# Kernel optimization log

Measured on AMD Instinct MI355X. Metric: run time of the kernel, lower is better.

## Reference

```python
import jax, jax.numpy as jnp
import numpy as np

D_MODEL = 512
D_INNER = 1024      # expand * d_model
NHEADS = 16         # d_inner // headdim, headdim = d_model // num_heads = 64
HEADDIM = 64
DSTATE = 64
DCONV = 4           # window_size
DFF = 2048
B, LM, LT = 16, 1024, 512


def _rmsnorm(x, eps=1e-6):
    return x * jax.lax.rsqrt(jnp.mean(x * x, axis=-1, keepdims=True) + eps)


def setup_inputs():
    key = jax.random.key(0)
    ks = jax.random.split(key, 10)
    conv_dim = D_INNER + 2 * DSTATE
    d_in_proj = 2 * D_INNER + 2 * DSTATE + NHEADS
    return {
        'tgt': jax.random.normal(ks[0], (B, LT, D_MODEL), jnp.float32),
        'memory': jax.random.normal(ks[1], (B, LM, D_MODEL), jnp.float32),
        'mem_mask': jnp.ones((B, LM), jnp.float32),
        'tgt_mask': jnp.ones((B, LT), jnp.float32),
        'in_proj_w': jax.random.normal(ks[2], (d_in_proj, D_MODEL), jnp.float32) * 0.02,
        'conv_w': jax.random.normal(ks[3], (conv_dim, DCONV), jnp.float32) * 0.2,
        'conv_b': jnp.zeros((conv_dim,), jnp.float32),
        'dt_bias': jax.random.uniform(ks[4], (NHEADS,), jnp.float32, -4.0, -2.0),
        'A_log': jnp.log(jax.random.uniform(ks[5], (NHEADS,), jnp.float32, 1.0, 16.0)),
        'D': jnp.ones((NHEADS,), jnp.float32),
        'norm_w': jnp.ones((D_INNER,), jnp.float32),
        'out_proj_w': jax.random.normal(ks[6], (D_MODEL, D_INNER), jnp.float32) * 0.02,
        'fc1_w': jax.random.normal(ks[7], (DFF, D_MODEL), jnp.float32) * 0.02,
        'fc1_b': jnp.zeros((DFF,), jnp.float32),
        'fc2_w': jax.random.normal(ks[8], (D_MODEL, DFF), jnp.float32) * 0.02,
        'fc2_b': jnp.zeros((D_MODEL,), jnp.float32),
    }


def _mamba2(u, in_proj_w, conv_w, conv_b, dt_bias, A_log, D, norm_w, out_proj_w):
    # u: (B, L, d_model) -- Mamba2-style selective scan (causal, ngroups=1)
    b, L, _ = u.shape
    zxbcdt = jnp.einsum('bld,ed->ble', u, in_proj_w)  # (B,L,2192)
    z = zxbcdt[..., :D_INNER]
    xBC = zxbcdt[..., D_INNER:D_INNER + D_INNER + 2 * DSTATE]
    dt = zxbcdt[..., -NHEADS:]

    # causal depthwise conv1d, kernel = DCONV, then swish
    xBC_pad = jnp.pad(xBC, ((0, 0), (DCONV - 1, 0), (0, 0)))
    conv = conv_b
    conv = sum(conv_w[:, k] * xBC_pad[:, k:k + L] for k in range(DCONV)) + conv_b
    xBC = jax.nn.silu(conv)

    x = xBC[..., :D_INNER].reshape(b, L, NHEADS, HEADDIM)   # (B,L,H,P)
    Bm = xBC[..., D_INNER:D_INNER + DSTATE]                  # (B,L,N)
    Cm = xBC[..., D_INNER + DSTATE:]                         # (B,L,N)

    dt = jax.nn.softplus(dt + dt_bias)                       # (B,L,H)
    A = -jnp.exp(A_log)                                      # (H,)
    a = jnp.exp(dt * A)                                      # (B,L,H) decay

    def step(h, inputs):
        a_t, dt_t, x_t, B_t, C_t = inputs
        # h: (B,H,P,N)
        h = a_t[:, :, None, None] * h + (dt_t[:, :, None] * x_t)[..., None] * B_t[:, None, None, :]
        y = jnp.einsum('bhpn,bn->bhp', h, C_t)
        return h, y

    h0 = jnp.zeros((b, NHEADS, HEADDIM, DSTATE), u.dtype)
    xs = (jnp.moveaxis(a, 1, 0), jnp.moveaxis(dt, 1, 0), jnp.moveaxis(x, 1, 0),
          jnp.moveaxis(Bm, 1, 0), jnp.moveaxis(Cm, 1, 0))
    _, ys = jax.lax.scan(step, h0, xs)                       # (L,B,H,P)
    y = jnp.moveaxis(ys, 0, 1) + D[None, None, :, None] * x  # skip term
    y = y.reshape(b, L, D_INNER)

    # gated RMSNorm + out_proj
    y = y * jax.nn.silu(z)
    y = _rmsnorm(y, 1e-5) * norm_w
    return jnp.einsum('ble,de->bld', y, out_proj_w)


def _forward(tgt, memory, mem_mask, tgt_mask, in_proj_w, conv_w, conv_b, dt_bias,
             A_log, D, norm_w, out_proj_w, fc1_w, fc1_b, fc2_w, fc2_b):
    tgt = tgt * tgt_mask[..., None]
    tgt1 = _rmsnorm(tgt)
    memory = memory * mem_mask[..., None]
    u = jnp.concatenate([memory, tgt1], axis=1)
    mask = jnp.concatenate([mem_mask, tgt_mask], axis=1)
    u = u * mask[..., None]
    tgt2 = _mamba2(u, in_proj_w, conv_w, conv_b, dt_bias, A_log, D, norm_w, out_proj_w)
    tgt2 = tgt2[:, -tgt1.shape[1]:]
    tgt = tgt + tgt2  # dropout = identity (eval)
    tgt1 = _rmsnorm(tgt)
    h = jax.nn.gelu(jnp.einsum('bld,fd->blf', tgt1, fc1_w) + fc1_b, approximate=False)
    tgt2 = jnp.einsum('blf,df->bld', h, fc2_w) + fc2_b
    return tgt + tgt2


def reference(tgt, memory, mem_mask, tgt_mask, in_proj_w, conv_w, conv_b, dt_bias,
              A_log, D, norm_w, out_proj_w, fc1_w, fc1_b, fc2_w, fc2_b):
    return _forward(tgt, memory, mem_mask, tgt_mask, in_proj_w, conv_w, conv_b, dt_bias,
                    A_log, D, norm_w, out_proj_w, fc1_w, fc1_b, fc2_w, fc2_b)
```

## Files before the change

### kernel.cpp

```cpp
#include <hip/hip_runtime.h>
#include <cstddef>

#define BB 16
#define LMM 1024
#define LTT 512
#define LL 1536
#define DMODEL 512
#define DINNER 1024
#define NH 16
#define DIPROJ 2192
#define DFF2 2048

typedef __bf16 bf16_t;
typedef bf16_t bf16x2 __attribute__((ext_vector_type(2)));
typedef bf16_t bf16x4 __attribute__((ext_vector_type(4)));
typedef bf16_t bf16x8 __attribute__((ext_vector_type(8)));
typedef float f32x4 __attribute__((ext_vector_type(4)));

typedef __attribute__((address_space(3))) void lds_void;
typedef const __attribute__((address_space(1))) void glb_void;

__device__ __forceinline__ void gload16(const void* g, void* l) {
  __builtin_amdgcn_global_load_lds((glb_void*)g, (lds_void*)l, 16, 0, 0);
}

__device__ inline float block_sum(float v, float* sbuf) {
#pragma unroll
  for (int off = 32; off > 0; off >>= 1) v += __shfl_xor(v, off, 64);
  int w = threadIdx.x >> 6;
  if ((threadIdx.x & 63) == 0) sbuf[w] = v;
  __syncthreads();
  return sbuf[0] + sbuf[1] + sbuf[2] + sbuf[3];
}

__global__ __launch_bounds__(256)
void cvt_w(const float* __restrict__ src, bf16_t* __restrict__ dst, int n)
{
  int i = (blockIdx.x * 256 + threadIdx.x) * 4;
  if (i < n) {
    float4 v = *(const float4*)&src[i];
    bf16x4 o;
    o[0] = (bf16_t)v.x; o[1] = (bf16_t)v.y; o[2] = (bf16_t)v.z; o[3] = (bf16_t)v.w;
    *(bf16x4*)&dst[i] = o;
  }
}

__global__ __launch_bounds__(256)
void prep_u(const float* __restrict__ tgt, const float* __restrict__ memory,
            const float* __restrict__ mem_mask, const float* __restrict__ tgt_mask,
            bf16_t* __restrict__ u, float* __restrict__ tgtm)
{
  __shared__ float sbuf[4];
  const int row = blockIdx.x;
  const int b = row / LL;
  const int t = row - b * LL;
  const int tid = threadIdx.x;
  if (t < LMM) {
    float m = mem_mask[b * LMM + t];
    float s = m * m;
    const float* src = memory + ((size_t)b * LMM + t) * DMODEL;
    float2 v = *(const float2*)&src[tid * 2];
    bf16x2 o; o[0] = (bf16_t)(v.x * s); o[1] = (bf16_t)(v.y * s);
    *(bf16x2*)&u[(size_t)row * DMODEL + tid * 2] = o;
  } else {
    const int tt = t - LMM;
    float mk = tgt_mask[b * LTT + tt];
    const float* src = tgt + ((size_t)b * LTT + tt) * DMODEL;
    float2 v = *(const float2*)&src[tid * 2];
    v.x *= mk; v.y *= mk;
    *(float2*)&tgtm[((size_t)b * LTT + tt) * DMODEL + tid * 2] = v;
    float ss = block_sum(v.x * v.x + v.y * v.y, sbuf);
    float inv = rsqrtf(ss * (1.0f / 512.0f) + 1e-6f) * mk;
    bf16x2 o; o[0] = (bf16_t)(v.x * inv); o[1] = (bf16_t)(v.y * inv);
    *(bf16x2*)&u[(size_t)row * DMODEL + tid * 2] = o;
  }
}

template<int EPI>
__global__ __launch_bounds__(256)
void gemm_abf(const bf16_t* __restrict__ A, const bf16_t* __restrict__ W,
              int M, int N, int K,
              float* __restrict__ Cf, bf16_t* __restrict__ Cb,
              const float* __restrict__ bias, const float* __restrict__ res,
              bf16_t* __restrict__ zbuf, bf16_t* __restrict__ xbc,
              float* __restrict__ dts, float* __restrict__ labuf,
              const float* __restrict__ dt_bias, const float* __restrict__ A_log)
{
  const int nbx = gridDim.x;
  const int nwg = nbx * gridDim.y;
  int flat = blockIdx.y * nbx + blockIdx.x;
  int swz = (flat & 7) * (nwg >> 3) + (flat >> 3);
  const int m0 = (swz / nbx) * 128;
  const int n0 = (swz % nbx) * 128;
  int bq = 0, tbase = 0;
  if (EPI == 4) {
    bq = m0 / LL; tbase = m0 - bq * LL;
    if (n0 + 128 <= DINNER && tbase < LMM) return;
  }
  __shared__ __align__(16) bf16_t As[2][128 * 64];
  __shared__ __align__(16) bf16_t Bs[2][128 * 64];
  const int tid = threadIdx.x;
  const int lane = tid & 63;
  const int wid = tid >> 6;
  const int wr = (wid >> 1) * 64, wc = (wid & 1) * 64;
  const int r = lane & 15;
  const int g = lane >> 4;
  const int r7 = r & 7;
  const int lrow = lane >> 3;
  const int sslot = (lane & 7) ^ lrow;

  int arow[4], brow[4];
#pragma unroll
  for (int ci = 0; ci < 4; ++ci) {
    int tr = wid * 32 + ci * 8 + lrow;
    arow[ci] = m0 + tr;
    int bn = n0 + tr;
    brow[ci] = bn < N ? bn : N - 1;
  }

  auto stage = [&](int buf, int kt) {
#pragma unroll
    for (int ci = 0; ci < 4; ++ci) {
      int chunk = wid * 4 + ci;
      gload16(A + (size_t)arow[ci] * K + kt + sslot * 8, &As[buf][chunk * 512]);
      gload16(W + (size_t)brow[ci] * K + kt + sslot * 8, &Bs[buf][chunk * 512]);
    }
  };

  f32x4 acc[4][4];
#pragma unroll
  for (int m = 0; m < 4; ++m)
#pragma unroll
    for (int n = 0; n < 4; ++n) acc[m][n] = (f32x4){0.f, 0.f, 0.f, 0.f};

  const int NK = K >> 6;
  stage(0, 0);
  __syncthreads();
  for (int ki = 0; ki < NK; ++ki) {
    const int cur = ki & 1;
    if (ki + 1 < NK) stage(cur ^ 1, (ki + 1) << 6);
#pragma unroll
    for (int c = 0; c < 2; ++c) {
      bf16x8 af[4], bfr[4];
#pragma unroll
      for (int m = 0; m < 4; ++m) {
        int row = wr + m * 16 + r;
        af[m] = *(const bf16x8*)&As[cur][row * 64 + (((c * 4 + g) ^ r7) * 8)];
      }
#pragma unroll
      for (int n = 0; n < 4; ++n) {
        int row = wc + n * 16 + r;
        bfr[n] = *(const bf16x8*)&Bs[cur][row * 64 + (((c * 4 + g) ^ r7) * 8)];
      }
#pragma unroll
      for (int m = 0; m < 4; ++m)
#pragma unroll
        for (int n = 0; n < 4; ++n)
          acc[m][n] = __builtin_amdgcn_mfma_f32_16x16x32_bf16(af[m], bfr[n], acc[m][n], 0, 0, 0);
    }
    if (ki + 1 < NK) __syncthreads();
  }

#pragma unroll
  for (int m = 0; m < 4; ++m) {
#pragma unroll
    for (int n = 0; n < 4; ++n) {
      int gcol = n0 + wc + n * 16 + r;
      if (gcol >= N) continue;
#pragma unroll
      for (int j = 0; j < 4; ++j) {
        float v = acc[m][n][j];
        if (EPI == 4) {
          int t = tbase + wr + m * 16 + g * 4 + j;
          if (gcol < DINNER) {
            zbuf[(((size_t)(bq * LTT + t - LMM)) << 10) + gcol] = (bf16_t)v;
          } else if (gcol < DINNER + 1152) {
            xbc[(size_t)(bq * LL + t) * 1152 + (gcol - DINNER)] = (bf16_t)v;
          } else {
            int h = gcol - 2176;
            float raw = v + dt_bias[h];
            float d = raw > 20.f ? raw : log1pf(expf(raw));
            size_t ix = (size_t)(bq * LL + t) * 16 + h;
            dts[ix] = d;
            labuf[ix] = -expf(A_log[h]) * d;
          }
        } else {
          int grow = m0 + wr + m * 16 + g * 4 + j;
          if (EPI == 1) {
            v += bias[gcol];
            v = 0.5f * v * (1.f + erff(v * 0.70710678f));
            Cb[(size_t)grow * N + gcol] = (bf16_t)v;
          } else if (EPI == 2) {
            v += bias[gcol] + res[(size_t)grow * N + gcol];
            Cf[(size_t)grow * N + gcol] = v;
          } else {
            v += res[(size_t)grow * N + gcol];
            Cf[(size_t)grow * N + gcol] = v;
          }
        }
      }
    }
  }
}

__global__ __launch_bounds__(256)
void sbc_k(const bf16_t* __restrict__ xbc, const float* __restrict__ cw,
           const float* __restrict__ cb, bf16_t* __restrict__ BtG,
           bf16_t* __restrict__ Sg, bf16_t* __restrict__ CcG)
{
  __shared__ __align__(16) bf16_t rawBC[132 * 128];
  __shared__ __align__(16) bf16_t CB[128 * 128];
  __shared__ float wls[128 * 4];
  __shared__ float bls[128];
  const int c = blockIdx.x, b = blockIdx.y;
  const int t0 = c * 128;
  const int tid = threadIdx.x, lane = tid & 63, wid = tid >> 6;
  const int r = lane & 15, g = lane >> 4;

  if (tid < 128) {
    int gch = 1024 + tid;
#pragma unroll
    for (int k = 0; k < 4; ++k) wls[tid * 4 + k] = cw[gch * 4 + k];
    bls[tid] = cb[gch];
  }
#pragma unroll
  for (int ci = 0; ci < 9; ++ci) {
    int chunk = ci * 4 + wid;
    if (chunk < 33) {
      int F = chunk * 1024 + lane * 16;
      int row = F >> 8, off = F & 255;
      gload16(xbc + (size_t)(b * LL + t0 - 3 + row) * 1152 + 1024 + off / 2,
              &rawBC[chunk * 512]);
    }
  }
  __syncthreads();
  if (c == 0 && tid < 48) {
    bf16x8 z;
#pragma unroll
    for (int j = 0; j < 8; ++j) z[j] = (bf16_t)0.f;
    *(bf16x8*)&rawBC[tid * 8] = z;
  }
  __syncthreads();
#pragma unroll 2
  for (int it = 0; it < 64; ++it) {
    int o = tid + it * 256;
    int t = o >> 7, ch = o & 127;
    float a0 = bls[ch];
#pragma unroll
    for (int kk = 0; kk < 4; ++kk)
      a0 = fmaf(wls[ch * 4 + kk], (float)rawBC[(t + kk) * 128 + ch], a0);
    float sv = a0 / (1.f + expf(-a0));
    int slot = ch >> 3;
    int swslot = (slot & 8) | ((slot & 7) ^ (t & 7));
    CB[t * 128 + swslot * 8 + (ch & 7)] = (bf16_t)sv;
    if (c >= 8 && ch >= 64) {
      int n = ch - 64;
      CcG[(((size_t)(b * 4 + (c - 8)) * 128 + t)) * 64 + (((n >> 3) ^ (t & 7)) << 3) + (n & 7)] = (bf16_t)sv;
    }
  }
  __syncthreads();
  {
    int n = tid & 63, tb = tid >> 6;
#pragma unroll
    for (int s8 = 0; s8 < 4; ++s8) {
      int ts = tb * 32 + s8 * 8;
      bf16x8 v;
#pragma unroll
      for (int e = 0; e < 8; ++e) {
        int t = ts + e;
        int slot = (n >> 3) ^ (t & 7);
        v[e] = CB[t * 128 + slot * 8 + (n & 7)];
      }
      *(bf16x8*)&BtG[((size_t)(b * 12 + c) * 64 + n) * 128 + ((((ts >> 3) ^ (n & 7))) << 3)] = v;
    }
  }
  if (c >= 8) {
    f32x4 sacc[2][8];
#pragma unroll
    for (int tt = 0; tt < 2; ++tt)
#pragma unroll
      for (int ct = 0; ct < 8; ++ct) sacc[tt][ct] = (f32x4){0.f, 0.f, 0.f, 0.f};
    const int ctn = 2 * wid + 2;
#pragma unroll
    for (int kk = 0; kk < 2; ++kk) {
      bf16x8 ca[2];
#pragma unroll
      for (int tt = 0; tt < 2; ++tt) {
        int trow = wid * 32 + tt * 16 + r;
        int slot = (64 + kk * 32 + g * 8) >> 3;
        int sw = (slot & 8) | ((slot & 7) ^ (trow & 7));
        ca[tt] = *(const bf16x8*)&CB[trow * 128 + sw * 8];
      }
#pragma unroll
      for (int ct = 0; ct < 8; ++ct) {
        if (ct < ctn) {
          int taur = ct * 16 + r;
          int sw = ((kk * 4 + g) ^ (taur & 7));
          bf16x8 bb = *(const bf16x8*)&CB[taur * 128 + sw * 8];
          sacc[0][ct] = __builtin_amdgcn_mfma_f32_16x16x32_bf16(ca[0], bb, sacc[0][ct], 0, 0, 0);
          sacc[1][ct] = __builtin_amdgcn_mfma_f32_16x16x32_bf16(ca[1], bb, sacc[1][ct], 0, 0, 0);
        }
      }
    }
    size_t sbase = (size_t)(b * 4 + (c - 8)) * 16384;
#pragma unroll
    for (int tt = 0; tt < 2; ++tt)
#pragma unroll
      for (int ct = 0; ct < 8; ++ct) {
        if (ct < ctn) {
#pragma unroll
          for (int j = 0; j < 4; ++j) {
            int ta = wid * 32 + tt * 16 + g * 4 + j;
            int tau = ct * 16 + r;
            Sg[sbase + ta * 128 + (tau ^ ((ta & 7) << 3))] = (bf16_t)sacc[tt][ct][j];
          }
        }
      }
  }
}

__global__ __launch_bounds__(256)
void ssd_hend(const bf16_t* __restrict__ xbc, const float* __restrict__ dts,
              const float* __restrict__ labuf, const float* __restrict__ cw,
              const float* __restrict__ cb, const bf16_t* __restrict__ BtG,
              bf16_t* __restrict__ hend, float* __restrict__ Lacum,
              float* __restrict__ Ak)
{
  __shared__ __align__(16) bf16_t rawX[136 * 64];
  __shared__ __align__(16) bf16_t Xt[64 * 128];
  __shared__ __align__(16) bf16_t Bt[64 * 128];
  __shared__ float wv[128];
  __shared__ float wls[64 * 4];
  __shared__ float bls[64];
  const int c = blockIdx.x;
  const int bh = blockIdx.y;
  const int b = bh >> 4, h = bh & 15;
  const int t0 = c * 128;
  const int tid = threadIdx.x, lane = tid & 63, wid = tid >> 6;
  const int r = lane & 15, g = lane >> 4;

  if (tid < 64) {
    int gch = h * 64 + tid;
#pragma unroll
    for (int k = 0; k < 4; ++k) wls[tid * 4 + k] = cw[gch * 4 + k];
    bls[tid] = cb[gch];
  }
#pragma unroll
  for (int ci = 0; ci < 5; ++ci) {
    int chunk = ci * 4 + wid;
    if (chunk < 17) {
      int F = chunk * 1024 + lane * 16;
      int row = F >> 7, off = F & 127;
      gload16(xbc + (size_t)(b * LL + t0 - 3 + row) * 1152 + h * 64 + off / 2,
              &rawX[chunk * 512]);
    }
  }
#pragma unroll
  for (int ci = 0; ci < 4; ++ci) {
    int chunk = ci * 4 + wid;
    int F = chunk * 1024 + lane * 16;
    gload16(BtG + (size_t)(b * 12 + c) * 8192 + F / 2, &Bt[chunk * 512]);
  }
  __syncthreads();
  if (c == 0 && tid < 24) {
    bf16x8 z;
#pragma unroll
    for (int j = 0; j < 8; ++j) z[j] = (bf16_t)0.f;
    *(bf16x8*)&rawX[tid * 8] = z;
  }
  if (tid < 64) {
    float v0 = labuf[(size_t)(b * LL + t0 + tid) * 16 + h];
    float v1 = labuf[(size_t)(b * LL + t0 + 64 + tid) * 16 + h];
    float d0 = dts[(size_t)(b * LL + t0 + tid) * 16 + h];
    float d1 = dts[(size_t)(b * LL + t0 + 64 + tid) * 16 + h];
#pragma unroll
    for (int d = 1; d < 64; d <<= 1) { float t_ = __shfl(v0, tid - d, 64); if (tid >= d) v0 += t_; }
    float T0 = __shfl(v0, 63, 64);
#pragma unroll
    for (int d = 1; d < 64; d <<= 1) { float t_ = __shfl(v1, tid - d, 64); if (tid >= d) v1 += t_; }
    v1 += T0;
    float Ls = __shfl(v1, 63, 64);
    wv[tid] = expf(Ls - v0) * d0; wv[64 + tid] = expf(Ls - v1) * d1;
    Lacum[(size_t)(bh * 12 + c) * 128 + tid] = v0;
    Lacum[(size_t)(bh * 12 + c) * 128 + 64 + tid] = v1;
    if (tid == 0) Ak[bh * 12 + c] = expf(Ls);
  }
  __syncthreads();
  {
    int p = tid & 63, tb = (tid >> 6) * 32;
    float w0 = wls[p * 4], w1 = wls[p * 4 + 1], w2 = wls[p * 4 + 2], w3 = wls[p * 4 + 3];
    float bb0 = bls[p];
    int sw = (p & 7) << 3;
#pragma unroll
    for (int i8 = 0; i8 < 4; ++i8) {
      bf16x8 ov;
#pragma unroll
      for (int e = 0; e < 8; ++e) {
        int t = tb + i8 * 8 + e;
        float a0 = bb0;
        a0 = fmaf(w0, (float)rawX[(t + 0) * 64 + p], a0);
        a0 = fmaf(w1, (float)rawX[(t + 1) * 64 + p], a0);
        a0 = fmaf(w2, (float)rawX[(t + 2) * 64 + p], a0);
        a0 = fmaf(w3, (float)rawX[(t + 3) * 64 + p], a0);
        ov[e] = (bf16_t)(a0 / (1.f + expf(-a0)));
      }
      *(bf16x8*)&Xt[p * 128 + ((tb + i8 * 8) ^ sw)] = ov;
    }
  }
  __syncthreads();
  f32x4 acc[4];
#pragma unroll
  for (int n = 0; n < 4; ++n) acc[n] = (f32x4){0.f, 0.f, 0.f, 0.f};
  const int prow = wid * 16 + r;
#pragma unroll
  for (int kk = 0; kk < 4; ++kk) {
    int k0 = kk * 32 + g * 8;
    bf16x8 xv = *(const bf16x8*)&Xt[prow * 128 + (k0 ^ ((prow & 7) << 3))];
    bf16x8 af;
#pragma unroll
    for (int j = 0; j < 8; ++j) af[j] = (bf16_t)((float)xv[j] * wv[k0 + j]);
#pragma unroll
    for (int nt = 0; nt < 4; ++nt) {
      int nrow = nt * 16 + r;
      bf16x8 bf_ = *(const bf16x8*)&Bt[nrow * 128 + (k0 ^ ((nrow & 7) << 3))];
      acc[nt] = __builtin_amdgcn_mfma_f32_16x16x32_bf16(af, bf_, acc[nt], 0, 0, 0);
    }
  }
  size_t base = ((size_t)(bh * 12 + c)) * 4096;
#pragma unroll
  for (int nt = 0; nt < 4; ++nt)
#pragma unroll
    for (int j = 0; j < 4; ++j)
      hend[base + (size_t)(wid * 16 + g * 4 + j) * 64 + nt * 16 + r] = (bf16_t)acc[nt][j];
}

__global__ __launch_bounds__(256)
void ssd_y(const bf16_t* __restrict__ xbc, const float* __restrict__ dts,
           const bf16_t* __restrict__ hend, const float* __restrict__ Ak,
           const float* __restrict__ Lacum, const bf16_t* __restrict__ Sg,
           const bf16_t* __restrict__ CcG, const float* __restrict__ cw,
           const float* __restrict__ cb, const float* __restrict__ Dp,
           bf16_t* __restrict__ ybuf)
{
  __shared__ __align__(16) char region0[32768];
  __shared__ __align__(16) bf16_t Xt[64 * 128];
  __shared__ __align__(16) bf16_t Cs[128 * 64];
  __shared__ __align__(16) bf16_t hts[64 * 64];
  __shared__ float Lat[128];
  __shared__ float dtv[128];
  __shared__ float wls[64 * 4];
  __shared__ float bls[64];
  bf16_t* rawX = (bf16_t*)region0;
  bf16_t* Gs   = (bf16_t*)region0;
  const int c = 8 + blockIdx.x;
  const int bh = blockIdx.y;
  const int b = bh >> 4, h = bh & 15;
  const int t0 = c * 128;
  const int tid = threadIdx.x, lane = tid & 63, wid = tid >> 6;
  const int r = lane & 15, g = lane >> 4;

  if (tid < 64) {
    int gch = h * 64 + tid;
#pragma unroll
    for (int k = 0; k < 4; ++k) wls[tid * 4 + k] = cw[gch * 4 + k];
    bls[tid] = cb[gch];
  }
  if (tid < 128) {
    Lat[tid] = Lacum[(size_t)(bh * 12 + c) * 128 + tid];
    dtv[tid] = dts[(size_t)(b * LL + t0 + tid) * 16 + h];
  }
#pragma unroll
  for (int ci = 0; ci < 5; ++ci) {
    int chunk = ci * 4 + wid;
    if (chunk < 17) {
      int F = chunk * 1024 + lane * 16;
      int row = F >> 7, off = F & 127;
      gload16(xbc + (size_t)(b * LL + t0 - 3 + row) * 1152 + h * 64 + off / 2,
              &rawX[chunk * 512]);
    }
  }
#pragma unroll
  for (int ci = 0; ci < 4; ++ci) {
    int chunk = ci * 4 + wid;
    int F = chunk * 1024 + lane * 16;
    gload16(CcG + (size_t)(b * 4 + (c - 8)) * 8192 + F / 2, &Cs[chunk * 512]);
  }
  {
    float hin[16];
#pragma unroll
    for (int e = 0; e < 16; ++e) hin[e] = 0.f;
    float accp = 1.f;
    for (int k = c - 1; k >= 0; --k) {
      const bf16_t* hp = hend + ((size_t)(bh * 12 + k)) * 4096 + tid * 16;
      bf16x8 e0 = *(const bf16x8*)hp;
      bf16x8 e1 = *(const bf16x8*)(hp + 8);
#pragma unroll
      for (int j = 0; j < 8; ++j) {
        hin[j]     = fmaf(accp, (float)e0[j], hin[j]);
        hin[j + 8] = fmaf(accp, (float)e1[j], hin[j + 8]);
      }
      accp *= Ak[bh * 12 + k];
    }
    int p = tid >> 2, n0 = (tid & 3) * 16;
    bf16x8 o0, o1;
#pragma unroll
    for (int j = 0; j < 8; ++j) { o0[j] = (bf16_t)hin[j]; o1[j] = (bf16_t)hin[j + 8]; }
    int p7 = p & 7;
    *(bf16x8*)&hts[p * 64 + (((n0 >> 3) ^ p7) << 3)] = o0;
    *(bf16x8*)&hts[p * 64 + ((((n0 >> 3) + 1) ^ p7) << 3)] = o1;
  }
  __syncthreads();
  {
    int p = tid & 63, tb = (tid >> 6) * 32;
    float w0 = wls[p * 4], w1 = wls[p * 4 + 1], w2 = wls[p * 4 + 2], w3 = wls[p * 4 + 3];
    float bb0 = bls[p];
    int sw = (p & 7) << 3;
#pragma unroll
    for (int i8 = 0; i8 < 4; ++i8) {
      bf16x8 ov;
#pragma unroll
      for (int e = 0; e < 8; ++e) {
        int t = tb + i8 * 8 + e;
        float a0 = bb0;
        a0 = fmaf(w0, (float)rawX[(t + 0) * 64 + p], a0);
        a0 = fmaf(w1, (float)rawX[(t + 1) * 64 + p], a0);
        a0 = fmaf(w2, (float)rawX[(t + 2) * 64 + p], a0);
        a0 = fmaf(w3, (float)rawX[(t + 3) * 64 + p], a0);
        ov[e] = (bf16_t)(a0 / (1.f + expf(-a0)));
      }
      *(bf16x8*)&Xt[p * 128 + ((tb + i8 * 8) ^ sw)] = ov;
    }
  }
  __syncthreads();
  {
    size_t sbase = (size_t)(b * 4 + (c - 8)) * 16384;
#pragma unroll
    for (int it = 0; it < 8; ++it) {
      int o = tid + it * 256;
      int ta = o >> 4, sl = o & 15;
      bf16x8 sv = *(const bf16x8*)&Sg[sbase + ta * 128 + sl * 8];
      int tau0 = (sl ^ (ta & 7)) * 8;
      float Lta = Lat[ta];
      bf16x8 gv;
#pragma unroll
      for (int e = 0; e < 8; ++e) {
        int tau = tau0 + e;
        float xa = (tau <= ta) ? (Lta - Lat[tau]) : -1e30f;
        gv[e] = (bf16_t)(expf(xa) * dtv[tau] * (float)sv[e]);
      }
      *(bf16x8*)&Gs[ta * 128 + sl * 8] = gv;
    }
  }
  __syncthreads();

  bf16x8 caf[2][2];
#pragma unroll
  for (int tt = 0; tt < 2; ++tt)
#pragma unroll
    for (int kk = 0; kk < 2; ++kk) {
      int trow = wid * 32 + tt * 16 + r;
      caf[tt][kk] = *(const bf16x8*)&Cs[trow * 64 + ((((kk * 4 + g)) ^ (trow & 7)) << 3)];
    }

  f32x4 accY[2][4], acc2[2][4];
#pragma unroll
  for (int tt = 0; tt < 2; ++tt)
#pragma unroll
    for (int pt = 0; pt < 4; ++pt) {
      accY[tt][pt] = (f32x4){0.f, 0.f, 0.f, 0.f};
      acc2[tt][pt] = (f32x4){0.f, 0.f, 0.f, 0.f};
    }
#pragma unroll
  for (int tt = 0; tt < 2; ++tt) {
    int trow = wid * 32 + tt * 16 + r;
#pragma unroll
    for (int kk = 0; kk < 4; ++kk) {
      if (kk <= wid) {
        int k0 = kk * 32 + g * 8;
        bf16x8 ga = *(const bf16x8*)&Gs[trow * 128 + (k0 ^ ((trow & 7) << 3))];
#pragma unroll
        for (int pt = 0; pt < 4; ++pt) {
          int prow = pt * 16 + r;
          bf16x8 xb = *(const bf16x8*)&Xt[prow * 128 + (k0 ^ ((prow & 7) << 3))];
          accY[tt][pt] = __builtin_amdgcn_mfma_f32_16x16x32_bf16(ga, xb, accY[tt][pt], 0, 0, 0);
        }
      }
    }
#pragma unroll
    for (int kk = 0; kk < 2; ++kk) {
#pragma unroll
      for (int pt = 0; pt < 4; ++pt) {
        int prow = pt * 16 + r;
        bf16x8 hb = *(const bf16x8*)&hts[prow * 64 + ((((kk * 4 + g)) ^ (prow & 7)) << 3)];
        acc2[tt][pt] = __builtin_amdgcn_mfma_f32_16x16x32_bf16(caf[tt][kk], hb, acc2[tt][pt], 0, 0, 0);
      }
    }
  }

  const float Dh = Dp[h];
#pragma unroll
  for (int tt = 0; tt < 2; ++tt) {
#pragma unroll
    for (int j = 0; j < 4; ++j) {
      int trow = wid * 32 + tt * 16 + g * 4 + j;
      float el = expf(Lat[trow]);
      size_t yrow = ((size_t)(b * LTT + (c - 8) * 128 + trow)) << 10;
#pragma unroll
      for (int pt = 0; pt < 4; ++pt) {
        int p = pt * 16 + r;
        float xv = (float)Xt[p * 128 + (trow ^ ((p & 7) << 3))];
        float yv = accY[tt][pt][j] + el * acc2[tt][pt][j] + Dh * xv;
        ybuf[yrow + h * 64 + p] = (bf16_t)yv;
      }
    }
  }
}

__global__ __launch_bounds__(256)
void gate_norm_k(const bf16_t* __restrict__ zbuf, const bf16_t* __restrict__ ybuf,
                 const float* __restrict__ norm_w, bf16_t* __restrict__ yn)
{
  __shared__ float sbuf[4];
  const int row = blockIdx.x;
  const int tid = threadIdx.x;
  bf16x4 yv = *(const bf16x4*)&ybuf[(size_t)row * DINNER + tid * 4];
  bf16x4 zv = *(const bf16x4*)&zbuf[(size_t)row * DINNER + tid * 4];
  float v[4];
#pragma unroll
  for (int c = 0; c < 4; ++c) {
    float y = (float)yv[c], z = (float)zv[c];
    v[c] = y * (z / (1.f + expf(-z)));
  }
  float ss = block_sum(v[0]*v[0] + v[1]*v[1] + v[2]*v[2] + v[3]*v[3], sbuf);
  float inv = rsqrtf(ss * (1.f / 1024.f) + 1e-5f);
  float4 nw = *(const float4*)&norm_w[tid * 4];
  bf16x4 o;
  o[0] = (bf16_t)(v[0] * inv * nw.x); o[1] = (bf16_t)(v[1] * inv * nw.y);
  o[2] = (bf16_t)(v[2] * inv * nw.z); o[3] = (bf16_t)(v[3] * inv * nw.w);
  *(bf16x4*)&yn[(size_t)row * DINNER + tid * 4] = o;
}

__global__ __launch_bounds__(256)
void rms_k(const float* __restrict__ in, bf16_t* __restrict__ out)
{
  __shared__ float sbuf[4];
  const int row = blockIdx.x;
  const int tid = threadIdx.x;
  float2 v = *(const float2*)&in[(size_t)row * DMODEL + tid * 2];
  float ss = block_sum(v.x * v.x + v.y * v.y, sbuf);
  float inv = rsqrtf(ss * (1.f / 512.f) + 1e-6f);
  bf16x2 o; o[0] = (bf16_t)(v.x * inv); o[1] = (bf16_t)(v.y * inv);
  *(bf16x2*)&out[(size_t)row * DMODEL + tid * 2] = o;
}

extern "C" void kernel_launch(void* const* d_in, const int* in_sizes, int n_in,
                              void* d_out, int out_size, void* d_ws, size_t ws_size,
                              hipStream_t stream)
{
  const float* tgt        = (const float*)d_in[0];
  const float* memory     = (const float*)d_in[1];
  const float* mem_mask   = (const float*)d_in[2];
  const float* tgt_mask   = (const float*)d_in[3];
  const float* in_proj_w  = (const float*)d_in[4];
  const float* conv_w     = (const float*)d_in[5];
  const float* conv_b     = (const float*)d_in[6];
  const float* dt_bias    = (const float*)d_in[7];
  const float* A_log      = (const float*)d_in[8];
  const float* Dp         = (const float*)d_in[9];
  const float* norm_w     = (const float*)d_in[10];
  const float* out_proj_w = (const float*)d_in[11];
  const float* fc1_w      = (const float*)d_in[12];
  const float* fc1_b      = (const float*)d_in[13];
  const float* fc2_w      = (const float*)d_in[14];
  const float* fc2_b      = (const float*)d_in[15];

  char* wsb = (char*)d_ws;
  bf16_t* u     = (bf16_t*)(wsb + 0);
  bf16_t* zbuf  = (bf16_t*)(wsb + 25165824);
  bf16_t* xbc   = (bf16_t*)(wsb + 41943040);
  float*  dts   = (float*)(wsb + 98566144);
  float*  labuf = (float*)(wsb + 100139008);
  float*  tgtm  = (float*)(wsb + 101711872);
  bf16_t* hend  = (bf16_t*)(wsb + 118489088);
  float*  Lacum = (float*)(wsb + 143667200);
  float*  Akb   = (float*)(wsb + 145240064);
  bf16_t* BtG   = (bf16_t*)(wsb + 145252352);
  bf16_t* Sg    = (bf16_t*)(wsb + 148398080);
  bf16_t* CcG   = (bf16_t*)(wsb + 150495232);
  bf16_t* wip   = (bf16_t*)(wsb + 160444416);
  bf16_t* wop   = wip + 1122304;
  bf16_t* wf1   = wop + 524288;
  bf16_t* wf2   = wf1 + 1048576;
  bf16_t* ybuf  = (bf16_t*)(wsb + 0);
  bf16_t* yn    = (bf16_t*)(wsb + 41943040);
  float*  tres  = (float*)(wsb + 58720256);
  bf16_t* t1    = (bf16_t*)(wsb + 75497472);
  bf16_t* hbuf  = (bf16_t*)(wsb + 0);
  float* outp = (float*)d_out;

  cvt_w<<<1096, 256, 0, stream>>>(in_proj_w, wip, 1122304);
  cvt_w<<<512, 256, 0, stream>>>(out_proj_w, wop, 524288);
  cvt_w<<<1024, 256, 0, stream>>>(fc1_w, wf1, 1048576);
  cvt_w<<<1024, 256, 0, stream>>>(fc2_w, wf2, 1048576);
  prep_u<<<BB * LL, 256, 0, stream>>>(tgt, memory, mem_mask, tgt_mask, u, tgtm);
  gemm_abf<4><<<dim3(18, 192), 256, 0, stream>>>(u, wip, BB * LL, DIPROJ, DMODEL,
      nullptr, nullptr, nullptr, nullptr, zbuf, xbc, dts, labuf, dt_bias, A_log);
  sbc_k<<<dim3(12, BB), 256, 0, stream>>>(xbc, conv_w, conv_b, BtG, Sg, CcG);
  ssd_hend<<<dim3(12, BB * NH), 256, 0, stream>>>(xbc, dts, labuf, conv_w, conv_b,
      BtG, hend, Lacum, Akb);
  ssd_y<<<dim3(4, BB * NH), 256, 0, stream>>>(xbc, dts, hend, Akb, Lacum, Sg, CcG,
      conv_w, conv_b, Dp, ybuf);
  gate_norm_k<<<BB * LTT, 256, 0, stream>>>(zbuf, ybuf, norm_w, yn);
  gemm_abf<3><<<dim3(4, 64), 256, 0, stream>>>(yn, wop, BB * LTT, DMODEL, DINNER,
      tres, nullptr, nullptr, tgtm, nullptr, nullptr, nullptr, nullptr, nullptr, nullptr);
  rms_k<<<BB * LTT, 256, 0, stream>>>(tres, t1);
  gemm_abf<1><<<dim3(16, 64), 256, 0, stream>>>(t1, wf1, BB * LTT, DFF2, DMODEL,
      nullptr, hbuf, fc1_b, nullptr, nullptr, nullptr, nullptr, nullptr, nullptr, nullptr);
  gemm_abf<2><<<dim3(4, 64), 256, 0, stream>>>(hbuf, wf2, BB * LTT, DMODEL, DFF2,
      outp, nullptr, fc2_b, tres, nullptr, nullptr, nullptr, nullptr, nullptr, nullptr);
}
```

Before: 338.6 us.

## Load GEMM fragments directly from global memory and merge weight conversion kernels

Replaces the LDS double-buffered GEMM staging with direct per-lane global loads of MFMA fragments, so shared memory and all __syncthreads disappear. The four weight-conversion launches become one kernel. A t>=LMM guard is added to the z-buffer write in the in_proj epilogue. Without LDS reuse, every wave fetches its A and B rows independently through cache, which raises global/L2 traffic and exposes memory latency with no explicit prefetching.

```diff
diff --git a/kernel.cpp b/kernel.cpp
--- a/kernel.cpp
+++ b/kernel.cpp
@@ -34,15 +34,22 @@
 }
 
 __global__ __launch_bounds__(256)
-void cvt_w(const float* __restrict__ src, bf16_t* __restrict__ dst, int n)
+void cvt_all(const float* __restrict__ s0, const float* __restrict__ s1,
+             const float* __restrict__ s2, const float* __restrict__ s3,
+             bf16_t* __restrict__ dst)
 {
   int i = (blockIdx.x * 256 + threadIdx.x) * 4;
-  if (i < n) {
-    float4 v = *(const float4*)&src[i];
-    bf16x4 o;
-    o[0] = (bf16_t)v.x; o[1] = (bf16_t)v.y; o[2] = (bf16_t)v.z; o[3] = (bf16_t)v.w;
-    *(bf16x4*)&dst[i] = o;
-  }
+  if (i >= 3743744) return;
+  const float* src;
+  int off;
+  if (i < 1122304)      { src = s0; off = i; }
+  else if (i < 1646592) { src = s1; off = i - 1122304; }
+  else if (i < 2695168) { src = s2; off = i - 1646592; }
+  else                  { src = s3; off = i - 2695168; }
+  float4 v = *(const float4*)&src[off];
+  bf16x4 o;
+  o[0] = (bf16_t)v.x; o[1] = (bf16_t)v.y; o[2] = (bf16_t)v.z; o[3] = (bf16_t)v.w;
+  *(bf16x4*)&dst[i] = o;
 }
 
 __global__ __launch_bounds__(256)
@@ -78,7 +85,7 @@
 
 template<int EPI>
 __global__ __launch_bounds__(256)
-void gemm_abf(const bf16_t* __restrict__ A, const bf16_t* __restrict__ W,
+void gemm_dir(const bf16_t* __restrict__ A, const bf16_t* __restrict__ W,
               int M, int N, int K,
               float* __restrict__ Cf, bf16_t* __restrict__ Cb,
               const float* __restrict__ bias, const float* __restrict__ res,
@@ -97,35 +104,24 @@
     bq = m0 / LL; tbase = m0 - bq * LL;
     if (n0 + 128 <= DINNER && tbase < LMM) return;
   }
-  __shared__ __align__(16) bf16_t As[2][128 * 64];
-  __shared__ __align__(16) bf16_t Bs[2][128 * 64];
   const int tid = threadIdx.x;
   const int lane = tid & 63;
   const int wid = tid >> 6;
   const int wr = (wid >> 1) * 64, wc = (wid & 1) * 64;
   const int r = lane & 15;
   const int g = lane >> 4;
-  const int r7 = r & 7;
-  const int lrow = lane >> 3;
-  const int sslot = (lane & 7) ^ lrow;
-
-  int arow[4], brow[4];
-#pragma unroll
-  for (int ci = 0; ci < 4; ++ci) {
-    int tr = wid * 32 + ci * 8 + lrow;
-    arow[ci] = m0 + tr;
-    int bn = n0 + tr;
-    brow[ci] = bn < N ? bn : N - 1;
-  }
-
-  auto stage = [&](int buf, int kt) {
-#pragma unroll
-    for (int ci = 0; ci < 4; ++ci) {
-      int chunk = wid * 4 + ci;
-      gload16(A + (size_t)arow[ci] * K + kt + sslot * 8, &As[buf][chunk * 512]);
-      gload16(W + (size_t)brow[ci] * K + kt + sslot * 8, &Bs[buf][chunk * 512]);
-    }
-  };
+
+  const bf16_t* ap[4];
+  const bf16_t* bp[4];
+#pragma unroll
+  for (int m = 0; m < 4; ++m)
+    ap[m] = A + (size_t)(m0 + wr + m * 16 + r) * K + g * 8;
+#pragma unroll
+  for (int n = 0; n < 4; ++n) {
+    int row = n0 + wc + n * 16 + r;
+    if (row >= N) row = N - 1;
+    bp[n] = W + (size_t)row * K + g * 8;
+  }
 
   f32x4 acc[4][4];
 #pragma unroll
@@ -133,32 +129,18 @@
 #pragma unroll
     for (int n = 0; n < 4; ++n) acc[m][n] = (f32x4){0.f, 0.f, 0.f, 0.f};
 
-  const int NK = K >> 6;
-  stage(0, 0);
-  __syncthreads();
-  for (int ki = 0; ki < NK; ++ki) {
-    const int cur = ki & 1;
-    if (ki + 1 < NK) stage(cur ^ 1, (ki + 1) << 6);
-#pragma unroll
-    for (int c = 0; c < 2; ++c) {
-      bf16x8 af[4], bfr[4];
-#pragma unroll
-      for (int m = 0; m < 4; ++m) {
-        int row = wr + m * 16 + r;
-        af[m] = *(const bf16x8*)&As[cur][row * 64 + (((c * 4 + g) ^ r7) * 8)];
-      }
-#pragma unroll
-      for (int n = 0; n < 4; ++n) {
-        int row = wc + n * 16 + r;
-        bfr[n] = *(const bf16x8*)&Bs[cur][row * 64 + (((c * 4 + g) ^ r7) * 8)];
-      }
-#pragma unroll
-      for (int m = 0; m < 4; ++m)
-#pragma unroll
-        for (int n = 0; n < 4; ++n)
-          acc[m][n] = __builtin_amdgcn_mfma_f32_16x16x32_bf16(af[m], bfr[n], acc[m][n], 0, 0, 0);
-    }
-    if (ki + 1 < NK) __syncthreads();
+#pragma unroll 2
+  for (int kt = 0; kt < K; kt += 32) {
+    bf16x8 af[4], bfr[4];
+#pragma unroll
+    for (int m = 0; m < 4; ++m) af[m] = *(const bf16x8*)(ap[m] + kt);
+#pragma unroll
+    for (int n = 0; n < 4; ++n) bfr[n] = *(const bf16x8*)(bp[n] + kt);
+#pragma unroll
+    for (int m = 0; m < 4; ++m)
+#pragma unroll
+      for (int n = 0; n < 4; ++n)
+        acc[m][n] = __builtin_amdgcn_mfma_f32_16x16x32_bf16(af[m], bfr[n], acc[m][n], 0, 0, 0);
   }
 
 #pragma unroll
@@ -173,7 +155,8 @@
         if (EPI == 4) {
           int t = tbase + wr + m * 16 + g * 4 + j;
           if (gcol < DINNER) {
-            zbuf[(((size_t)(bq * LTT + t - LMM)) << 10) + gcol] = (bf16_t)v;
+            if (t >= LMM)
+              zbuf[(((size_t)(bq * LTT + t - LMM)) << 10) + gcol] = (bf16_t)v;
           } else if (gcol < DINNER + 1152) {
             xbc[(size_t)(bq * LL + t) * 1152 + (gcol - DINNER)] = (bf16_t)v;
           } else {
@@ -698,12 +681,9 @@
   bf16_t* hbuf  = (bf16_t*)(wsb + 0);
   float* outp = (float*)d_out;
 
-  cvt_w<<<1096, 256, 0, stream>>>(in_proj_w, wip, 1122304);
-  cvt_w<<<512, 256, 0, stream>>>(out_proj_w, wop, 524288);
-  cvt_w<<<1024, 256, 0, stream>>>(fc1_w, wf1, 1048576);
-  cvt_w<<<1024, 256, 0, stream>>>(fc2_w, wf2, 1048576);
+  cvt_all<<<3656, 256, 0, stream>>>(in_proj_w, out_proj_w, fc1_w, fc2_w, wip);
   prep_u<<<BB * LL, 256, 0, stream>>>(tgt, memory, mem_mask, tgt_mask, u, tgtm);
-  gemm_abf<4><<<dim3(18, 192), 256, 0, stream>>>(u, wip, BB * LL, DIPROJ, DMODEL,
+  gemm_dir<4><<<dim3(18, 192), 256, 0, stream>>>(u, wip, BB * LL, DIPROJ, DMODEL,
       nullptr, nullptr, nullptr, nullptr, zbuf, xbc, dts, labuf, dt_bias, A_log);
   sbc_k<<<dim3(12, BB), 256, 0, stream>>>(xbc, conv_w, conv_b, BtG, Sg, CcG);
   ssd_hend<<<dim3(12, BB * NH), 256, 0, stream>>>(xbc, dts, labuf, conv_w, conv_b,
@@ -711,11 +691,11 @@
   ssd_y<<<dim3(4, BB * NH), 256, 0, stream>>>(xbc, dts, hend, Akb, Lacum, Sg, CcG,
       conv_w, conv_b, Dp, ybuf);
   gate_norm_k<<<BB * LTT, 256, 0, stream>>>(zbuf, ybuf, norm_w, yn);
-  gemm_abf<3><<<dim3(4, 64), 256, 0, stream>>>(yn, wop, BB * LTT, DMODEL, DINNER,
+  gemm_dir<3><<<dim3(4, 64), 256, 0, stream>>>(yn, wop, BB * LTT, DMODEL, DINNER,
       tres, nullptr, nullptr, tgtm, nullptr, nullptr, nullptr, nullptr, nullptr, nullptr);
   rms_k<<<BB * LTT, 256, 0, stream>>>(tres, t1);
-  gemm_abf<1><<<dim3(16, 64), 256, 0, stream>>>(t1, wf1, BB * LTT, DFF2, DMODEL,
+  gemm_dir<1><<<dim3(16, 64), 256, 0, stream>>>(t1, wf1, BB * LTT, DFF2, DMODEL,
       nullptr, hbuf, fc1_b, nullptr, nullptr, nullptr, nullptr, nullptr, nullptr, nullptr);
-  gemm_abf<2><<<dim3(4, 64), 256, 0, stream>>>(hbuf, wf2, BB * LTT, DMODEL, DFF2,
+  gemm_dir<2><<<dim3(4, 64), 256, 0, stream>>>(hbuf, wf2, BB * LTT, DMODEL, DFF2,
       outp, nullptr, fc2_b, tres, nullptr, nullptr, nullptr, nullptr, nullptr, nullptr);
 }
```

After: 469.5 us. 38.7% more time.
